# Optimization experiments

Hardware: AMD Instinct MI355X
Metric: run time of the kernel (lower is better)

The kernel has to match this reference:

```python
import jax, jax.numpy as jnp
import numpy as np

HEADDIM = 128
CHUNK = 256


def _ssd_scan(x, dt, A, B, C, chunk):
    # x: (b,l,h,p)  dt: (b,l,h)  A: (h,)  B,C: (b,l,n)  (single group g=1 shared by all heads)
    b, l, h, p = x.shape
    n = B.shape[-1]
    nc = l // chunk
    dA = dt * A  # (b,l,h)
    xc = x.reshape(b, nc, chunk, h, p)
    dtc = dt.reshape(b, nc, chunk, h)
    dAc = dA.reshape(b, nc, chunk, h)
    Bc = B.reshape(b, nc, chunk, n)
    Cc = C.reshape(b, nc, chunk, n)
    cs = jnp.cumsum(dAc, axis=2)  # (b,nc,c,h) cumulative log-decay within chunk
    # intra-chunk quadratic part
    CB = jnp.einsum('bjin,bjkn->bjik', Cc, Bc)  # (b,nc,c,c)
    decay = jnp.exp(cs[:, :, :, None, :] - cs[:, :, None, :, :])  # (b,nc,i,k,h)
    mask = jnp.tril(jnp.ones((chunk, chunk), dtype=bool))
    decay = jnp.where(mask[None, None, :, :, None], decay, 0.0)
    y_intra = jnp.einsum('bjik,bjikh,bjkh,bjkhp->bjihp', CB, decay, dtc, xc)
    # per-chunk end states
    decay_states = jnp.exp(cs[:, :, -1:, :] - cs)  # (b,nc,c,h)
    states = jnp.einsum('bjkh,bjkh,bjkn,bjkhp->bjhnp', decay_states, dtc, Bc, xc)
    # recurrence across chunks: h_j = exp(sum dA_j) * h_{j-1} + states_j
    chunk_decay = jnp.exp(cs[:, :, -1, :])  # (b,nc,h)
    def step(carry, inp):
        s, d = inp
        new = carry * d[:, :, None, None] + s
        return new, carry  # emit state BEFORE this chunk
    init = jnp.zeros((b, h, n, p), x.dtype)
    _, prev = jax.lax.scan(step, init,
                           (states.transpose(1, 0, 2, 3, 4), chunk_decay.transpose(1, 0, 2)))
    prev = prev.transpose(1, 0, 2, 3, 4)  # (b,nc,h,n,p)
    y_inter = jnp.einsum('bjih,bjin,bjhnp->bjihp', jnp.exp(cs), Cc, prev)
    return (y_intra + y_inter).reshape(b, l, h, p)


def setup_inputs() -> dict:
    key = jax.random.key(0)
    k1, k2, k3, k4 = jax.random.split(key, 4)
    b, l, d_inner, nheads, d_state = 2, 4096, 2048, 16, 256
    x = jax.random.normal(k1, (b, l, d_inner), dtype=jnp.float32)
    BC = jax.random.normal(k2, (b, l, 2 * d_state), dtype=jnp.float32) * 0.1
    dt = jax.random.normal(k3, (b, l, 2 * nheads), dtype=jnp.float32) - 3.0
    A_log = jnp.zeros((nheads,), dtype=jnp.float32)
    D = jnp.ones((nheads,), dtype=jnp.float32)
    W_fcD = jax.random.normal(k4, (nheads, d_inner), dtype=jnp.float32) * 0.02
    return {"x": x, "BC": BC, "dt": dt, "A_log": A_log, "D": D, "W_fcD": W_fcD}


def reference(x, BC, dt, A_log, D, W_fcD):
    b, l, dim = x.shape
    h = A_log.shape[0]
    p = HEADDIM
    d_state = BC.shape[-1] // 2
    A = -jnp.exp(A_log)
    # bidirectional: concat forward stream with time-flipped backward stream along batch
    dt2 = jnp.concatenate((dt[:, :, :h], jnp.flip(dt[:, :, h:], axis=1)), axis=0)
    dt2 = jax.nn.softplus(dt2)
    x_og = x
    x2 = jnp.concatenate((x, jnp.flip(x, axis=1)), axis=0)
    BC2 = jnp.concatenate((BC, jnp.flip(BC, axis=1)), axis=0)
    B, C = BC2[..., :d_state], BC2[..., d_state:]
    y = _ssd_scan(x2.reshape(2 * b, l, h, p), dt2, A, B, C, CHUNK)
    y = y.reshape(2 * b, l, dim)
    y = jnp.roll(y, shift=1, axis=1).at[:, 0, :].set(0.0)
    y_fw, y_bw = y[:b], jnp.flip(y[b:], axis=1)
    gate = x_og @ W_fcD.T + D  # (b,l,h)
    y = y_fw + y_bw + x_og * jnp.repeat(gate, p, axis=-1)
    return y
```

## Files before the change

### kernel.cpp

```cpp
#include <hip/hip_runtime.h>
#include <stdint.h>

#define NB 2
#define SL 4096
#define NH 16
#define HD 128
#define DS 256
#define CK 256
#define NCH 16
#define NSQ 4
#define DI 2048

#define EPST 132

typedef unsigned short u16;
typedef unsigned int u32;
typedef __attribute__((ext_vector_type(8))) __bf16 bf16x8;
typedef __attribute__((ext_vector_type(4))) float f32x4;

__device__ __forceinline__ int tor(int dir, int t) { return dir ? (SL - 1 - t) : t; }

__device__ __forceinline__ u16 f2bf(float f) {
  u32 u = __float_as_uint(f);
  u = u + 0x7fffu + ((u >> 16) & 1u);
  return (u16)(u >> 16);
}
__device__ __forceinline__ float bf2f(u16 s) {
  return __uint_as_float(((u32)s) << 16);
}

struct Stg { uint4 a, b; };

__device__ __forceinline__ Stg ld_tile(const u16* __restrict__ src, int row, int q0, int k0) {
  const uint4* p = (const uint4*)(src + (size_t)row * 256 + k0 + (q0 << 3));
  Stg s; s.a = p[0]; s.b = p[1]; return s;
}
__device__ __forceinline__ void st_tile(u16* buf, int row, int q0, Stg s) {
  int sw = (row >> 1) & 3;
  *(uint4*)&buf[row * 32 + ((q0 ^ sw) << 3)] = s.a;
  *(uint4*)&buf[row * 32 + (((q0 + 1) ^ sw) << 3)] = s.b;
}

__device__ __forceinline__ bf16x8 frag(const u16* lds, int base_row, int m, int quad) {
  int row = base_row + m;
  return *(const bf16x8*)&lds[row * 32 + ((quad ^ ((row >> 1) & 3)) << 3)];
}

__device__ __forceinline__ void mfma16(const u16* As, const u16* Bs, int wi, int wp,
                                       int m, int quad, f32x4 acc[4][4]) {
  bf16x8 af[4], bv[4];
#pragma unroll
  for (int r = 0; r < 4; ++r) af[r] = frag(As, wi + (r << 4), m, quad);
#pragma unroll
  for (int c = 0; c < 4; ++c) bv[c] = frag(Bs, wp + (c << 4), m, quad);
#pragma unroll
  for (int r = 0; r < 4; ++r)
#pragma unroll
    for (int c = 0; c < 4; ++c)
      acc[r][c] = __builtin_amdgcn_mfma_f32_16x16x32_bf16(af[r], bv[c], acc[r][c], 0, 0, 0);
}

__global__ __launch_bounds__(256) void kprep(const float* __restrict__ dt,
                                             const float* __restrict__ A_log,
                                             float* __restrict__ csb,
                                             float* __restrict__ dtvb,
                                             float* __restrict__ cdecb) {
  int blk = blockIdx.x;
  int h = blk & 15, sj = blk >> 4;
  int s = sj >> 4, j = sj & 15;
  int b = s & 1, dir = s >> 1;
  int i = threadIdx.x;
  int to = tor(dir, j * CK + i);
  __shared__ float sbuf[CK];
  float a = -expf(A_log[h]);
  float raw = dt[((size_t)(b * SL + to)) * (2 * NH) + dir * NH + h];
  float sp = (raw > 20.f) ? raw : log1pf(expf(raw));
  sbuf[i] = sp * a;
  __syncthreads();
  for (int off = 1; off < CK; off <<= 1) {
    float v = (i >= off) ? sbuf[i - off] : 0.f;
    __syncthreads();
    sbuf[i] += v;
    __syncthreads();
  }
  float csv = sbuf[i];
  size_t base = ((size_t)sj * NH + h) * CK;
  csb[base + i] = csv;
  dtvb[base + i] = sp;
  if (i == CK - 1) cdecb[sj * NH + h] = expf(csv);
}

__global__ __launch_bounds__(256) void kcast(const float* __restrict__ BC,
                                             u16* __restrict__ Bbf,
                                             u16* __restrict__ Cbf) {
  int blk = blockIdx.x;
  int s = blk >> 12, t = blk & (SL - 1);
  int b = s & 1, dir = s >> 1;
  int tsrc = tor(dir, t);
  int tid = threadIdx.x;
  const float* src = BC + ((size_t)(b * SL + tsrc)) * (2 * DS);
  size_t dstb = ((size_t)s * SL + t) * DS;
  Bbf[dstb + tid] = f2bf(src[tid]);
  Cbf[dstb + tid] = f2bf(src[DS + tid]);
}

__global__ __launch_bounds__(256) void ktransB(const u16* __restrict__ Bbf,
                                               u16* __restrict__ BbfT) {
  int sj = blockIdx.x;
  int s = sj >> 4, j = sj & 15;
  __shared__ u16 T[64 * 264];
  int tid = threadIdx.x;
  const u16* src = Bbf + ((size_t)s * SL + j * CK) * DS;
  u16* dst = BbfT + (size_t)sj * DS * CK;
  int kr = tid >> 2, part = (tid & 3) * 64;
  for (int k0 = 0; k0 < CK; k0 += 64) {
    __syncthreads();
    {
      const uint4* gs = (const uint4*)(src + (size_t)(k0 + kr) * DS + part);
      uint4* tb = (uint4*)&T[kr * 264 + part];
#pragma unroll
      for (int q = 0; q < 8; ++q) tb[q] = gs[q];
    }
    __syncthreads();
    int n = tid;
    u16 col[64];
#pragma unroll
    for (int kq = 0; kq < 64; ++kq) col[kq] = T[kq * 264 + n];
    uint4* ds_ = (uint4*)(dst + (size_t)n * CK + k0);
#pragma unroll
    for (int q = 0; q < 8; ++q) {
      uint4 wv;
      wv.x = (u32)col[q * 8 + 0] | ((u32)col[q * 8 + 1] << 16);
      wv.y = (u32)col[q * 8 + 2] | ((u32)col[q * 8 + 3] << 16);
      wv.z = (u32)col[q * 8 + 4] | ((u32)col[q * 8 + 5] << 16);
      wv.w = (u32)col[q * 8 + 6] | ((u32)col[q * 8 + 7] << 16);
      ds_[q] = wv;
    }
  }
}

__global__ __launch_bounds__(256) void kxsT(const float* __restrict__ xg,
                                            const float* __restrict__ csb,
                                            const float* __restrict__ dtvb,
                                            u16* __restrict__ xsT) {
  int inst = blockIdx.x;
  int h = inst & 15, sj = inst >> 4;
  int s = sj >> 4, j = sj & 15;
  int b = s & 1, dir = s >> 1;
  int tid = threadIdx.x;
  __shared__ u16 Ls[128 * 40];
  size_t cbase = ((size_t)sj * NH + h) * CK;
  u16* dst = xsT + (size_t)inst * (128 * 256);
  int kk = tid >> 3;
  int pg = (tid & 7) * 16;
  int p2 = tid >> 1, half = tid & 1;
  float4 v[4];
  {
    int t = tor(dir, j * CK + kk);
    const float* src = xg + ((size_t)(b * SL + t)) * DI + h * HD + pg;
    v[0] = ((const float4*)src)[0]; v[1] = ((const float4*)src)[1];
    v[2] = ((const float4*)src)[2]; v[3] = ((const float4*)src)[3];
  }
  for (int k0 = 0; k0 < CK; k0 += 32) {
    int kglob = k0 + kk;
    float sc_ = expf(-csb[cbase + kglob]) * dtvb[cbase + kglob];
    float vv[16] = {v[0].x, v[0].y, v[0].z, v[0].w, v[1].x, v[1].y, v[1].z, v[1].w,
                    v[2].x, v[2].y, v[2].z, v[2].w, v[3].x, v[3].y, v[3].z, v[3].w};
    __syncthreads();
#pragma unroll
    for (int q = 0; q < 16; ++q) Ls[(pg + q) * 40 + kk] = f2bf(vv[q] * sc_);
    if (k0 + 32 < CK) {
      int t = tor(dir, j * CK + k0 + 32 + kk);
      const float* src = xg + ((size_t)(b * SL + t)) * DI + h * HD + pg;
      v[0] = ((const float4*)src)[0]; v[1] = ((const float4*)src)[1];
      v[2] = ((const float4*)src)[2]; v[3] = ((const float4*)src)[3];
    }
    __syncthreads();
    uint4 w0 = *(const uint4*)&Ls[p2 * 40 + half * 16];
    uint4 w1 = *(const uint4*)&Ls[p2 * 40 + half * 16 + 8];
    *(uint4*)&dst[(size_t)p2 * 256 + k0 + half * 16] = w0;
    *(uint4*)&dst[(size_t)p2 * 256 + k0 + half * 16 + 8] = w1;
  }
}

__global__ __launch_bounds__(256) void kcb(const u16* __restrict__ Cbf,
                                           const u16* __restrict__ Bbf,
                                           u16* __restrict__ CBm) {
  int blk = blockIdx.x;
  int tri = blk % 3;
  int sj = blk / 3;
  int it0 = tri ? 128 : 0;
  int kt0 = (tri == 2) ? 128 : 0;
  int s = sj >> 4, j = sj & 15;
  __shared__ u16 smem[128 * EPST];
  int tid = threadIdx.x;
  int w = tid >> 6, lane = tid & 63;
  int wi = (w >> 1) << 6, wp = (w & 1) << 6;
  int m = lane & 15, quad = lane >> 4;
  int row = tid >> 1, q0 = (tid & 1) << 1;
  const u16* Ab = Cbf + ((size_t)s * SL + j * CK + it0) * DS;
  const u16* Bb = Bbf + ((size_t)s * SL + j * CK + kt0) * DS;
  f32x4 zini = {0.f, 0.f, 0.f, 0.f};
  f32x4 acc[4][4];
#pragma unroll
  for (int r = 0; r < 4; ++r)
#pragma unroll
    for (int c = 0; c < 4; ++c) acc[r][c] = zini;
  const int n = 8;
  Stg pa = ld_tile(Ab, row, q0, 0);
  Stg pb = ld_tile(Bb, row, q0, 0);
  st_tile(smem, row, q0, pa);
  st_tile(smem + 8192, row, q0, pb);
  pa = ld_tile(Ab, row, q0, 32);
  pb = ld_tile(Bb, row, q0, 32);
  for (int ks = 1; ks < n; ++ks) {
    __syncthreads();
    int cur = (ks & 1) << 12;
    st_tile(smem + cur, row, q0, pa);
    st_tile(smem + 8192 + cur, row, q0, pb);
    if (ks + 1 < n) {
      pa = ld_tile(Ab, row, q0, (ks + 1) << 5);
      pb = ld_tile(Bb, row, q0, (ks + 1) << 5);
    }
    int prv = ((ks - 1) & 1) << 12;
    mfma16(smem + prv, smem + 8192 + prv, wi, wp, m, quad, acc);
  }
  __syncthreads();
  {
    int prv = ((n - 1) & 1) << 12;
    mfma16(smem + prv, smem + 8192 + prv, wi, wp, m, quad, acc);
  }
  __syncthreads();
  int diag = (it0 == kt0);
#pragma unroll
  for (int r = 0; r < 4; ++r)
#pragma unroll
    for (int rg = 0; rg < 4; ++rg) {
      int irow = wi + (r << 4) + (quad << 2) + rg;
#pragma unroll
      for (int c = 0; c < 4; ++c) {
        int kcol = wp + (c << 4) + m;
        float v = acc[r][c][rg];
        if (diag && kcol > irow) v = 0.f;
        smem[irow * EPST + kcol] = f2bf(v);
      }
    }
  __syncthreads();
  {
    u16* dstb = CBm + ((size_t)sj * CK + it0) * CK + kt0;
    int rr = tid >> 1, off = (tid & 1) << 6;
    const uint4* srcv = (const uint4*)&smem[rr * EPST + off];
    uint4* dstv = (uint4*)(dstb + (size_t)rr * CK + off);
#pragma unroll
    for (int q = 0; q < 8; ++q) dstv[q] = srcv[q];
  }
}

__global__ __launch_bounds__(256) void kstates(const u16* __restrict__ xsT,
                                               const u16* __restrict__ BbfT,
                                               const float* __restrict__ cdecb,
                                               u16* __restrict__ prevT) {
  int blk = blockIdx.x;
  int ntile = blk & 1;
  int inst = blk >> 1;
  int h = inst & 15, sj = inst >> 4;
  int nt0 = ntile << 7;
  __shared__ u16 smem[128 * EPST];
  int tid = threadIdx.x;
  int w = tid >> 6, lane = tid & 63;
  int wi = (w >> 1) << 6, wp = (w & 1) << 6;
  int m = lane & 15, quad = lane >> 4;
  int row = tid >> 1, q0 = (tid & 1) << 1;
  const u16* Ab = xsT + (size_t)inst * (128 * 256);
  const u16* Bb = BbfT + ((size_t)sj * DS + nt0) * CK;
  f32x4 zini = {0.f, 0.f, 0.f, 0.f};
  f32x4 acc[4][4];
#pragma unroll
  for (int r = 0; r < 4; ++r)
#pragma unroll
    for (int c = 0; c < 4; ++c) acc[r][c] = zini;
  const int n = 8;
  Stg pa = ld_tile(Ab, row, q0, 0);
  Stg pb = ld_tile(Bb, row, q0, 0);
  st_tile(smem, row, q0, pa);
  st_tile(smem + 8192, row, q0, pb);
  pa = ld_tile(Ab, row, q0, 32);
  pb = ld_tile(Bb, row, q0, 32);
  for (int ks = 1; ks < n; ++ks) {
    __syncthreads();
    int cur = (ks & 1) << 12;
    st_tile(smem + cur, row, q0, pa);
    st_tile(smem + 8192 + cur, row, q0, pb);
    if (ks + 1 < n) {
      pa = ld_tile(Ab, row, q0, (ks + 1) << 5);
      pb = ld_tile(Bb, row, q0, (ks + 1) << 5);
    }
    int prv = ((ks - 1) & 1) << 12;
    mfma16(smem + prv, smem + 8192 + prv, wi, wp, m, quad, acc);
  }
  __syncthreads();
  {
    int prv = ((n - 1) & 1) << 12;
    mfma16(smem + prv, smem + 8192 + prv, wi, wp, m, quad, acc);
  }
  __syncthreads();
  float scale = cdecb[sj * NH + h];
#pragma unroll
  for (int r = 0; r < 4; ++r)
#pragma unroll
    for (int rg = 0; rg < 4; ++rg) {
      int prow = wi + (r << 4) + (quad << 2) + rg;
#pragma unroll
      for (int c = 0; c < 4; ++c) {
        int ncol = wp + (c << 4) + m;
        smem[prow * EPST + ncol] = f2bf(acc[r][c][rg] * scale);
      }
    }
  __syncthreads();
  {
    u16* dstb = prevT + (size_t)inst * (128 * 256) + nt0;
    int rr = tid >> 1, off = (tid & 1) << 6;
    const uint4* srcv = (const uint4*)&smem[rr * EPST + off];
    uint4* dstv = (uint4*)(dstb + (size_t)rr * 256 + off);
#pragma unroll
    for (int q = 0; q < 8; ++q) dstv[q] = srcv[q];
  }
}

__global__ __launch_bounds__(256) void kscan(u16* __restrict__ prevT,
                                             const float* __restrict__ cdecb) {
  int g = blockIdx.x * 256 + threadIdx.x;
  int n0 = (g & 31) * 8;
  int p = (g >> 5) & 127;
  int h = (g >> 12) & 15;
  int s = g >> 16;
  size_t base = ((size_t)(s * 256 + h) * 128 + p) * 256 + n0;
  const size_t stride = (size_t)NH * 128 * 256;
  float carry[8] = {0.f, 0.f, 0.f, 0.f, 0.f, 0.f, 0.f, 0.f};
  uint4 u = *(const uint4*)&prevT[base];
  for (int j = 0; j < NCH; ++j) {
    size_t idx = base + (size_t)j * stride;
    uint4 un;
    if (j + 1 < NCH) un = *(const uint4*)&prevT[idx + stride];
    u32 uu[4] = {u.x, u.y, u.z, u.w};
    float sv[8];
#pragma unroll
    for (int q = 0; q < 4; ++q) {
      sv[2 * q] = __uint_as_float(uu[q] << 16);
      sv[2 * q + 1] = __uint_as_float(uu[q] & 0xffff0000u);
    }
    uint4 wv;
    wv.x = (u32)f2bf(carry[0]) | ((u32)f2bf(carry[1]) << 16);
    wv.y = (u32)f2bf(carry[2]) | ((u32)f2bf(carry[3]) << 16);
    wv.z = (u32)f2bf(carry[4]) | ((u32)f2bf(carry[5]) << 16);
    wv.w = (u32)f2bf(carry[6]) | ((u32)f2bf(carry[7]) << 16);
    *(uint4*)&prevT[idx] = wv;
    float d = cdecb[(s * NCH + j) * NH + h];
#pragma unroll
    for (int q = 0; q < 8; ++q) carry[q] = carry[q] * d + sv[q];
    u = un;
  }
}

__global__ __launch_bounds__(256) void ky(const u16* __restrict__ CBm,
                                          const u16* __restrict__ Cbf,
                                          const u16* __restrict__ xsT,
                                          const u16* __restrict__ prevT,
                                          const float* __restrict__ csb,
                                          u16* __restrict__ ytmpb) {
  int blk = blockIdx.x;
  int itile = blk & 1;
  int inst = blk >> 1;
  int h = inst & 15, sj = inst >> 4;
  int s = sj >> 4, j = sj & 15;
  int it0 = itile << 7;
  __shared__ u16 smem[128 * EPST];
  int tid = threadIdx.x;
  int w = tid >> 6, lane = tid & 63;
  int wi = (w >> 1) << 6, wp = (w & 1) << 6;
  int m = lane & 15, quad = lane >> 4;
  int row = tid >> 1, q0 = (tid & 1) << 1;

  const u16* Ai = CBm + ((size_t)sj * CK + it0) * CK;
  const u16* Ae = Cbf + ((size_t)s * SL + j * CK + it0) * DS;
  const u16* Bi = xsT + (size_t)inst * (128 * 256);
  const u16* Be = prevT + (size_t)inst * (128 * 256);

  int nIntra = itile ? 8 : 4;
  int n = nIntra + 8;

  f32x4 zini = {0.f, 0.f, 0.f, 0.f};
  f32x4 acc[4][4];
#pragma unroll
  for (int r = 0; r < 4; ++r)
#pragma unroll
    for (int c = 0; c < 4; ++c) acc[r][c] = zini;

#define KY_SRC(ks, Ap, Bp, kk)                                  \
  {                                                             \
    int intra_ = (ks) < nIntra;                                 \
    kk = (intra_ ? (ks) : (ks) - nIntra) << 5;                  \
    Ap = intra_ ? Ai : Ae;                                      \
    Bp = intra_ ? Bi : Be;                                      \
  }

  const u16 *Ap, *Bp; int kk;
  KY_SRC(0, Ap, Bp, kk);
  Stg pa = ld_tile(Ap, row, q0, kk);
  Stg pb = ld_tile(Bp, row, q0, kk);
  st_tile(smem, row, q0, pa);
  st_tile(smem + 8192, row, q0, pb);
  KY_SRC(1, Ap, Bp, kk);
  pa = ld_tile(Ap, row, q0, kk);
  pb = ld_tile(Bp, row, q0, kk);
  for (int ks = 1; ks < n; ++ks) {
    __syncthreads();
    int cur = (ks & 1) << 12;
    st_tile(smem + cur, row, q0, pa);
    st_tile(smem + 8192 + cur, row, q0, pb);
    if (ks + 1 < n) {
      KY_SRC(ks + 1, Ap, Bp, kk);
      pa = ld_tile(Ap, row, q0, kk);
      pb = ld_tile(Bp, row, q0, kk);
    }
    int prv = ((ks - 1) & 1) << 12;
    mfma16(smem + prv, smem + 8192 + prv, wi, wp, m, quad, acc);
  }
  __syncthreads();
  {
    int prv = ((n - 1) & 1) << 12;
    mfma16(smem + prv, smem + 8192 + prv, wi, wp, m, quad, acc);
  }
  __syncthreads();
#undef KY_SRC

  const float* csrow = csb + ((size_t)sj * NH + h) * CK + it0;
#pragma unroll
  for (int r = 0; r < 4; ++r)
#pragma unroll
    for (int rg = 0; rg < 4; ++rg) {
      int irow = wi + (r << 4) + (quad << 2) + rg;
      float esc = expf(csrow[irow]);
#pragma unroll
      for (int c = 0; c < 4; ++c) {
        int pcol = wp + (c << 4) + m;
        smem[irow * EPST + pcol] = f2bf(acc[r][c][rg] * esc);
      }
    }
  __syncthreads();
  {
    u16* yb = ytmpb + ((size_t)s * SL + j * CK + it0) * DI + h * HD;
    int rr = tid >> 1, off = (tid & 1) << 6;
    const uint4* srcv = (const uint4*)&smem[rr * EPST + off];
    uint4* dstv = (uint4*)(yb + (size_t)rr * DI + off);
#pragma unroll
    for (int q = 0; q < 8; ++q) dstv[q] = srcv[q];
  }
}

__global__ __launch_bounds__(256) void kwt(const float* __restrict__ Wg,
                                           float* __restrict__ WT) {
  int g = blockIdx.x * 256 + threadIdx.x;
  int d = g >> 4, h = g & 15;
  WT[g] = Wg[(size_t)h * DI + d];
}

__global__ __launch_bounds__(256) void kgate(const float* __restrict__ xg,
                                             const float* __restrict__ WT,
                                             const float* __restrict__ Dg,
                                             float* __restrict__ gate) {
  int wave = (blockIdx.x * 256 + threadIdx.x) >> 6;
  int lane = threadIdx.x & 63;
  int gg = lane >> 4, h = lane & 15;
  int row0 = wave * 8;
  const float* xb = xg + (size_t)row0 * DI;
  float acc[8] = {0.f, 0.f, 0.f, 0.f, 0.f, 0.f, 0.f, 0.f};
  for (int q = 0; q < 128; ++q) {
    int d = gg * 4 + 16 * q;
    float w0 = WT[(d + 0) * 16 + h];
    float w1 = WT[(d + 1) * 16 + h];
    float w2 = WT[(d + 2) * 16 + h];
    float w3 = WT[(d + 3) * 16 + h];
#pragma unroll
    for (int r = 0; r < 8; ++r) {
      float4 xv = *(const float4*)&xb[(size_t)r * DI + d];
      acc[r] += xv.x * w0 + xv.y * w1 + xv.z * w2 + xv.w * w3;
    }
  }
#pragma unroll
  for (int r = 0; r < 8; ++r) {
    acc[r] += __shfl_down(acc[r], 32);
    acc[r] += __shfl_down(acc[r], 16);
  }
  if (lane < 16) {
    float dv = Dg[h];
#pragma unroll
    for (int r = 0; r < 8; ++r) gate[(size_t)(row0 + r) * NH + h] = acc[r] + dv;
  }
}

__device__ __forceinline__ void unpk8(uint4 u, float* o) {
  o[0] = __uint_as_float(u.x << 16); o[1] = __uint_as_float(u.x & 0xffff0000u);
  o[2] = __uint_as_float(u.y << 16); o[3] = __uint_as_float(u.y & 0xffff0000u);
  o[4] = __uint_as_float(u.z << 16); o[5] = __uint_as_float(u.z & 0xffff0000u);
  o[6] = __uint_as_float(u.w << 16); o[7] = __uint_as_float(u.w & 0xffff0000u);
}

__global__ __launch_bounds__(256) void kcombine(const float* __restrict__ xg,
                                                const float* __restrict__ gate,
                                                const u16* __restrict__ ytmpb,
                                                float* __restrict__ out) {
  int bid = blockIdx.x;
  int b = bid >> 12;
  int t = bid & (SL - 1);
  int tid = threadIdx.x;
  int d0 = tid * 8;
  float g = gate[(size_t)(b * SL + t) * NH + (tid >> 4)];
  float fy[8] = {0.f, 0.f, 0.f, 0.f, 0.f, 0.f, 0.f, 0.f};
  float by[8] = {0.f, 0.f, 0.f, 0.f, 0.f, 0.f, 0.f, 0.f};
  if (t > 0) {
    uint4 u = *(const uint4*)(ytmpb + ((size_t)(b * SL + (t - 1))) * DI + d0);
    unpk8(u, fy);
  }
  if (t < SL - 1) {
    uint4 u = *(const uint4*)(ytmpb + ((size_t)((2 + b) * SL + (SL - 2 - t))) * DI + d0);
    unpk8(u, by);
  }
  const float* xr = xg + ((size_t)(b * SL + t)) * DI + d0;
  float4 x0 = ((const float4*)xr)[0];
  float4 x1 = ((const float4*)xr)[1];
  float xa[8] = {x0.x, x0.y, x0.z, x0.w, x1.x, x1.y, x1.z, x1.w};
  float* op = out + ((size_t)(b * SL + t)) * DI + d0;
  float4 o0, o1;
  o0.x = fy[0] + by[0] + xa[0] * g; o0.y = fy[1] + by[1] + xa[1] * g;
  o0.z = fy[2] + by[2] + xa[2] * g; o0.w = fy[3] + by[3] + xa[3] * g;
  o1.x = fy[4] + by[4] + xa[4] * g; o1.y = fy[5] + by[5] + xa[5] * g;
  o1.z = fy[6] + by[6] + xa[6] * g; o1.w = fy[7] + by[7] + xa[7] * g;
  ((float4*)op)[0] = o0;
  ((float4*)op)[1] = o1;
}

extern "C" void kernel_launch(void* const* d_in, const int* in_sizes, int n_in,
                              void* d_out, int out_size, void* d_ws, size_t ws_size,
                              hipStream_t stream) {
  (void)in_sizes; (void)n_in; (void)out_size; (void)ws_size;
  const float* x     = (const float*)d_in[0];
  const float* BC    = (const float*)d_in[1];
  const float* dt    = (const float*)d_in[2];
  const float* A_log = (const float*)d_in[3];
  const float* Dg    = (const float*)d_in[4];
  const float* W     = (const float*)d_in[5];
  float* out = (float*)d_out;

  char* p = (char*)d_ws;
  float* cs   = (float*)p;  p += (size_t)NSQ * NCH * NH * CK * 4;
  float* dtv  = (float*)p;  p += (size_t)NSQ * NCH * NH * CK * 4;
  float* cdec = (float*)p;  p += (size_t)NSQ * NCH * NH * 4;
  float* WT   = (float*)p;  p += (size_t)DI * NH * 4;
  float* gateb= (float*)p;  p += (size_t)NB * SL * NH * 4;
  u16* Bbf    = (u16*)p;    p += (size_t)NSQ * SL * DS * 2;
  u16* Cbf    = (u16*)p;    p += (size_t)NSQ * SL * DS * 2;
  u16* BbfT   = (u16*)p;    p += (size_t)NSQ * NCH * DS * CK * 2;
  u16* CBm    = (u16*)p;    p += (size_t)NSQ * NCH * CK * CK * 2;
  u16* xsT    = (u16*)p;    p += (size_t)NSQ * NCH * NH * HD * CK * 2;
  u16* prevT  = (u16*)p;    p += (size_t)NSQ * NCH * NH * HD * DS * 2;
  u16* ytmpb  = (u16*)p;    p += (size_t)NSQ * SL * DI * 2;

  hipLaunchKernelGGL(kprep,   dim3(NSQ * NCH * NH),      dim3(CK),  0, stream, dt, A_log, cs, dtv, cdec);
  hipLaunchKernelGGL(kcast,   dim3(NSQ * SL),            dim3(256), 0, stream, BC, Bbf, Cbf);
  hipLaunchKernelGGL(ktransB, dim3(NSQ * NCH),           dim3(256), 0, stream, Bbf, BbfT);
  hipLaunchKernelGGL(kxsT,    dim3(NSQ * NCH * NH),      dim3(256), 0, stream, x, cs, dtv, xsT);
  hipLaunchKernelGGL(kcb,     dim3(NSQ * NCH * 3),       dim3(256), 0, stream, Cbf, Bbf, CBm);
  hipLaunchKernelGGL(kwt,     dim3(DI * NH / 256),       dim3(256), 0, stream, W, WT);
  hipLaunchKernelGGL(kgate,   dim3(NB * SL / 32),        dim3(256), 0, stream, x, WT, Dg, gateb);
  hipLaunchKernelGGL(kstates, dim3(NSQ * NCH * NH * 2),  dim3(256), 0, stream, xsT, BbfT, cdec, prevT);
  hipLaunchKernelGGL(kscan,   dim3(NSQ * NH * HD * DS / (256 * 8)), dim3(256), 0, stream, prevT, cdec);
  hipLaunchKernelGGL(ky,      dim3(NSQ * NCH * NH * 2),  dim3(256), 0, stream, CBm, Cbf, xsT, prevT, cs, ytmpb);
  hipLaunchKernelGGL(kcombine,dim3(NB * SL),             dim3(256), 0, stream, x, gateb, ytmpb, out);
}
```

Measured before the change: 418.6 us.

## Fuse BC cast with B transpose and deepen GEMM global prefetch to two stages

The separate cast and B-transpose kernels become one kernel that converts a 64-row slab of B/C to bf16, writes the row-major copies, and transposes B through shared memory in the same block. This removes one launch and the re-read of B from global memory. The three MFMA GEMM kernels (kcb, kstates, ky) now keep two register-staged tiles in flight instead of one, to hide more global load latency at the cost of extra registers. The kcb launch is also moved ahead of kxsT.

Result: no change. 421.6 us (+0.7%).

```diff
diff --git a/kernel.cpp b/kernel.cpp
--- a/kernel.cpp
+++ b/kernel.cpp
@@ -90,52 +90,51 @@
   if (i == CK - 1) cdecb[sj * NH + h] = expf(csv);
 }
 
-__global__ __launch_bounds__(256) void kcast(const float* __restrict__ BC,
-                                             u16* __restrict__ Bbf,
-                                             u16* __restrict__ Cbf) {
+__global__ __launch_bounds__(256) void kcastT(const float* __restrict__ BC,
+                                              u16* __restrict__ Bbf,
+                                              u16* __restrict__ Cbf,
+                                              u16* __restrict__ BbfT) {
   int blk = blockIdx.x;
-  int s = blk >> 12, t = blk & (SL - 1);
+  int kq = blk & 3, sj = blk >> 2;
+  int s = sj >> 4, j = sj & 15;
   int b = s & 1, dir = s >> 1;
+  __shared__ u16 T[64 * 264];
+  int tid = threadIdx.x;
+  int r = tid >> 2, part = (tid & 3) * 64;
+  int t = j * CK + kq * 64 + r;
   int tsrc = tor(dir, t);
-  int tid = threadIdx.x;
   const float* src = BC + ((size_t)(b * SL + tsrc)) * (2 * DS);
   size_t dstb = ((size_t)s * SL + t) * DS;
-  Bbf[dstb + tid] = f2bf(src[tid]);
-  Cbf[dstb + tid] = f2bf(src[DS + tid]);
-}
-
-__global__ __launch_bounds__(256) void ktransB(const u16* __restrict__ Bbf,
-                                               u16* __restrict__ BbfT) {
-  int sj = blockIdx.x;
-  int s = sj >> 4, j = sj & 15;
-  __shared__ u16 T[64 * 264];
-  int tid = threadIdx.x;
-  const u16* src = Bbf + ((size_t)s * SL + j * CK) * DS;
-  u16* dst = BbfT + (size_t)sj * DS * CK;
-  int kr = tid >> 2, part = (tid & 3) * 64;
-  for (int k0 = 0; k0 < CK; k0 += 64) {
-    __syncthreads();
-    {
-      const uint4* gs = (const uint4*)(src + (size_t)(k0 + kr) * DS + part);
-      uint4* tb = (uint4*)&T[kr * 264 + part];
-#pragma unroll
-      for (int q = 0; q < 8; ++q) tb[q] = gs[q];
-    }
-    __syncthreads();
-    int n = tid;
-    u16 col[64];
-#pragma unroll
-    for (int kq = 0; kq < 64; ++kq) col[kq] = T[kq * 264 + n];
-    uint4* ds_ = (uint4*)(dst + (size_t)n * CK + k0);
-#pragma unroll
-    for (int q = 0; q < 8; ++q) {
-      uint4 wv;
-      wv.x = (u32)col[q * 8 + 0] | ((u32)col[q * 8 + 1] << 16);
-      wv.y = (u32)col[q * 8 + 2] | ((u32)col[q * 8 + 3] << 16);
-      wv.z = (u32)col[q * 8 + 4] | ((u32)col[q * 8 + 5] << 16);
-      wv.w = (u32)col[q * 8 + 6] | ((u32)col[q * 8 + 7] << 16);
-      ds_[q] = wv;
-    }
+  u16 bb[64], cc[64];
+#pragma unroll
+  for (int q = 0; q < 16; ++q) {
+    float4 v = ((const float4*)(src + part))[q];
+    bb[q * 4 + 0] = f2bf(v.x); bb[q * 4 + 1] = f2bf(v.y);
+    bb[q * 4 + 2] = f2bf(v.z); bb[q * 4 + 3] = f2bf(v.w);
+    float4 c = ((const float4*)(src + DS + part))[q];
+    cc[q * 4 + 0] = f2bf(c.x); cc[q * 4 + 1] = f2bf(c.y);
+    cc[q * 4 + 2] = f2bf(c.z); cc[q * 4 + 3] = f2bf(c.w);
+  }
+#pragma unroll
+  for (int q = 0; q < 8; ++q) {
+    ((uint4*)(Bbf + dstb + part))[q] = *(const uint4*)&bb[q * 8];
+    ((uint4*)(Cbf + dstb + part))[q] = *(const uint4*)&cc[q * 8];
+    *(uint4*)&T[r * 264 + part + q * 8] = *(const uint4*)&bb[q * 8];
+  }
+  __syncthreads();
+  int n = tid;
+  u16 col[64];
+#pragma unroll
+  for (int kk = 0; kk < 64; ++kk) col[kk] = T[kk * 264 + n];
+  uint4* ds_ = (uint4*)(BbfT + (size_t)sj * DS * CK + (size_t)n * CK + kq * 64);
+#pragma unroll
+  for (int q = 0; q < 8; ++q) {
+    uint4 wv;
+    wv.x = (u32)col[q * 8 + 0] | ((u32)col[q * 8 + 1] << 16);
+    wv.y = (u32)col[q * 8 + 2] | ((u32)col[q * 8 + 3] << 16);
+    wv.z = (u32)col[q * 8 + 4] | ((u32)col[q * 8 + 5] << 16);
+    wv.w = (u32)col[q * 8 + 6] | ((u32)col[q * 8 + 7] << 16);
+    ds_[q] = wv;
   }
 }
 
@@ -211,16 +210,19 @@
   Stg pb = ld_tile(Bb, row, q0, 0);
   st_tile(smem, row, q0, pa);
   st_tile(smem + 8192, row, q0, pb);
-  pa = ld_tile(Ab, row, q0, 32);
-  pb = ld_tile(Bb, row, q0, 32);
+  Stg a1 = ld_tile(Ab, row, q0, 32);
+  Stg b1 = ld_tile(Bb, row, q0, 32);
+  Stg a2 = ld_tile(Ab, row, q0, 64);
+  Stg b2 = ld_tile(Bb, row, q0, 64);
   for (int ks = 1; ks < n; ++ks) {
     __syncthreads();
     int cur = (ks & 1) << 12;
-    st_tile(smem + cur, row, q0, pa);
-    st_tile(smem + 8192 + cur, row, q0, pb);
-    if (ks + 1 < n) {
-      pa = ld_tile(Ab, row, q0, (ks + 1) << 5);
-      pb = ld_tile(Bb, row, q0, (ks + 1) << 5);
+    st_tile(smem + cur, row, q0, a1);
+    st_tile(smem + 8192 + cur, row, q0, b1);
+    a1 = a2; b1 = b2;
+    if (ks + 2 < n) {
+      a2 = ld_tile(Ab, row, q0, (ks + 2) << 5);
+      b2 = ld_tile(Bb, row, q0, (ks + 2) << 5);
     }
     int prv = ((ks - 1) & 1) << 12;
     mfma16(smem + prv, smem + 8192 + prv, wi, wp, m, quad, acc);
@@ -284,16 +286,19 @@
   Stg pb = ld_tile(Bb, row, q0, 0);
   st_tile(smem, row, q0, pa);
   st_tile(smem + 8192, row, q0, pb);
-  pa = ld_tile(Ab, row, q0, 32);
-  pb = ld_tile(Bb, row, q0, 32);
+  Stg a1 = ld_tile(Ab, row, q0, 32);
+  Stg b1 = ld_tile(Bb, row, q0, 32);
+  Stg a2 = ld_tile(Ab, row, q0, 64);
+  Stg b2 = ld_tile(Bb, row, q0, 64);
   for (int ks = 1; ks < n; ++ks) {
     __syncthreads();
     int cur = (ks & 1) << 12;
-    st_tile(smem + cur, row, q0, pa);
-    st_tile(smem + 8192 + cur, row, q0, pb);
-    if (ks + 1 < n) {
-      pa = ld_tile(Ab, row, q0, (ks + 1) << 5);
-      pb = ld_tile(Bb, row, q0, (ks + 1) << 5);
+    st_tile(smem + cur, row, q0, a1);
+    st_tile(smem + 8192 + cur, row, q0, b1);
+    a1 = a2; b1 = b2;
+    if (ks + 2 < n) {
+      a2 = ld_tile(Ab, row, q0, (ks + 2) << 5);
+      b2 = ld_tile(Bb, row, q0, (ks + 2) << 5);
     }
     int prv = ((ks - 1) & 1) << 12;
     mfma16(smem + prv, smem + 8192 + prv, wi, wp, m, quad, acc);
@@ -411,17 +416,21 @@
   st_tile(smem, row, q0, pa);
   st_tile(smem + 8192, row, q0, pb);
   KY_SRC(1, Ap, Bp, kk);
-  pa = ld_tile(Ap, row, q0, kk);
-  pb = ld_tile(Bp, row, q0, kk);
+  Stg a1 = ld_tile(Ap, row, q0, kk);
+  Stg b1 = ld_tile(Bp, row, q0, kk);
+  KY_SRC(2, Ap, Bp, kk);
+  Stg a2 = ld_tile(Ap, row, q0, kk);
+  Stg b2 = ld_tile(Bp, row, q0, kk);
   for (int ks = 1; ks < n; ++ks) {
     __syncthreads();
     int cur = (ks & 1) << 12;
-    st_tile(smem + cur, row, q0, pa);
-    st_tile(smem + 8192 + cur, row, q0, pb);
-    if (ks + 1 < n) {
-      KY_SRC(ks + 1, Ap, Bp, kk);
-      pa = ld_tile(Ap, row, q0, kk);
-      pb = ld_tile(Bp, row, q0, kk);
+    st_tile(smem + cur, row, q0, a1);
+    st_tile(smem + 8192 + cur, row, q0, b1);
+    a1 = a2; b1 = b2;
+    if (ks + 2 < n) {
+      KY_SRC(ks + 2, Ap, Bp, kk);
+      a2 = ld_tile(Ap, row, q0, kk);
+      b2 = ld_tile(Bp, row, q0, kk);
     }
     int prv = ((ks - 1) & 1) << 12;
     mfma16(smem + prv, smem + 8192 + prv, wi, wp, m, quad, acc);
@@ -567,10 +576,9 @@
   u16* ytmpb  = (u16*)p;    p += (size_t)NSQ * SL * DI * 2;
 
   hipLaunchKernelGGL(kprep,   dim3(NSQ * NCH * NH),      dim3(CK),  0, stream, dt, A_log, cs, dtv, cdec);
-  hipLaunchKernelGGL(kcast,   dim3(NSQ * SL),            dim3(256), 0, stream, BC, Bbf, Cbf);
-  hipLaunchKernelGGL(ktransB, dim3(NSQ * NCH),           dim3(256), 0, stream, Bbf, BbfT);
+  hipLaunchKernelGGL(kcastT,  dim3(NSQ * NCH * 4),       dim3(256), 0, stream, BC, Bbf, Cbf, BbfT);
+  hipLaunchKernelGGL(kcb,     dim3(NSQ * NCH * 3),       dim3(256), 0, stream, Cbf, Bbf, CBm);
   hipLaunchKernelGGL(kxsT,    dim3(NSQ * NCH * NH),      dim3(256), 0, stream, x, cs, dtv, xsT);
-  hipLaunchKernelGGL(kcb,     dim3(NSQ * NCH * 3),       dim3(256), 0, stream, Cbf, Bbf, CBm);
   hipLaunchKernelGGL(kwt,     dim3(DI * NH / 256),       dim3(256), 0, stream, W, WT);
   hipLaunchKernelGGL(kgate,   dim3(NB * SL / 32),        dim3(256), 0, stream, x, WT, Dg, gateb);
   hipLaunchKernelGGL(kstates, dim3(NSQ * NCH * NH * 2),  dim3(256), 0, stream, xsT, BbfT, cdec, prevT);
```
